# Optimization experiments

Hardware: AMD Instinct MI355X
Metric: run time of the kernel (lower is better)

## Reference

```python
import jax, jax.numpy as jnp
import numpy as np

N = 100000   # nodes
E = 1600000  # edges
D = 128      # input_dim
H = 128      # hidden_dim
O = 64       # output_dim


def setup_inputs() -> dict:
    key = jax.random.key(0)
    ks = jax.random.split(key, 10)
    x = jax.random.normal(ks[0], (N, D), dtype=jnp.float32)
    edge_index = jax.random.randint(ks[1], (2, E), 0, N, dtype=jnp.int32)

    def glorot(k, fan_in, fan_out):
        lim = np.sqrt(6.0 / (fan_in + fan_out)).astype(np.float32)
        return jax.random.uniform(k, (fan_in, fan_out), jnp.float32, -lim, lim)

    return {
        "x": x,
        "edge_index": edge_index,
        "W0": glorot(ks[2], D, H), "b0": jnp.zeros((H,), jnp.float32),
        "W1": glorot(ks[3], H, H), "b1": jnp.zeros((H,), jnp.float32),
        "W2": glorot(ks[4], H, H), "b2": jnp.zeros((H,), jnp.float32),
        "W3": glorot(ks[5], H, O), "b3": jnp.zeros((O,), jnp.float32),
    }


def gcn_conv(x, src, dst, W, b):
    """PyG GCNConv: out = D^{-1/2} (A + I) D^{-1/2} (x W) + b."""
    n = x.shape[0]
    h = x @ W                                # [N, out]
    loop = jnp.arange(n, dtype=src.dtype)    # self loops
    s = jnp.concatenate([src, loop])
    d = jnp.concatenate([dst, loop])
    deg = jax.ops.segment_sum(jnp.ones_like(d, dtype=h.dtype), d, num_segments=n)
    dinv = jax.lax.rsqrt(jnp.maximum(deg, 1.0))  # deg >= 1 because of self loops
    norm = dinv[s] * dinv[d]                     # [E+N]
    out = jax.ops.segment_sum(h[s] * norm[:, None], d, num_segments=n)
    return out + b


def reference(x, edge_index, W0, b0, W1, b1, W2, b2, W3, b3):
    src, dst = edge_index[0], edge_index[1]
    # three GCNBlocks: GCNConv + ReLU (dropout disabled)
    h = jax.nn.relu(gcn_conv(x, src, dst, W0, b0))
    h = jax.nn.relu(gcn_conv(h, src, dst, W1, b1))
    h = jax.nn.relu(gcn_conv(h, src, dst, W2, b2))
    # final bare GCNConv -> output_dim (no activation)
    return gcn_conv(h, src, dst, W3, b3)
```

## Files before the change

### kernel.cpp

```cpp
#include <hip/hip_runtime.h>
#include <math.h>

#define NN 100000
#define NE 1600000
#define NB 391

typedef __attribute__((ext_vector_type(8))) short short8;
typedef __attribute__((ext_vector_type(4))) float f32x4;
union frag8 { short s[8]; short8 v; };

__device__ __forceinline__ void split_bf16(float a, short& hi, short& lo) {
    unsigned u = __float_as_uint(a);
    unsigned hb = u & 0xffff0000u;
    hi = (short)(hb >> 16);
    float r = a - __uint_as_float(hb);
    unsigned lu = __float_as_uint(r);
    lo = (short)((lu + 0x7fff + ((lu >> 16) & 1)) >> 16);
}

__global__ __launch_bounds__(256) void hist_k(const int* __restrict__ dst, int* __restrict__ hist, int e) {
    __shared__ int h[NB];
    int t = threadIdx.x;
    for (int i = t; i < NB; i += 256) h[i] = 0;
    __syncthreads();
    int base = blockIdx.x * 4096;
#pragma unroll
    for (int j = 0; j < 16; ++j) {
        int i = base + j * 256 + t;
        if (i < e) atomicAdd(&h[dst[i] >> 8], 1);
    }
    __syncthreads();
    for (int i = t; i < NB; i += 256) if (h[i]) atomicAdd(&hist[i], h[i]);
}

__global__ __launch_bounds__(512) void bktscan_k(const int* __restrict__ hist,
                                                 int* __restrict__ boff, int* __restrict__ bcur) {
    __shared__ int wsum[8];
    int t = threadIdx.x, lane = t & 63, wid = t >> 6;
    int v = (t < NB) ? hist[t] : 0;
    int inc = v;
#pragma unroll
    for (int off = 1; off < 64; off <<= 1) {
        int tt = __shfl_up(inc, off);
        if (lane >= off) inc += tt;
    }
    if (lane == 63) wsum[wid] = inc;
    __syncthreads();
    int woff = 0;
    for (int w = 0; w < wid; ++w) woff += wsum[w];
    int excl = inc - v + woff;
    if (t < NB) { boff[t] = excl; bcur[t] = excl; }
    if (t == NB - 1) boff[NB] = excl + v;
}

__global__ __launch_bounds__(256) void part2_k(const int* __restrict__ src, const int* __restrict__ dst,
                                               int* bcur, int2* __restrict__ pairs, int e) {
    __shared__ int lhist[NB];
    __shared__ int lbase[NB];
    int t = threadIdx.x;
    for (int i = t; i < NB; i += 256) lhist[i] = 0;
    __syncthreads();
    int e0 = blockIdx.x * 4096;
    int sreg[16], dreg[16];
#pragma unroll
    for (int j = 0; j < 16; ++j) {
        int i = e0 + j * 256 + t;
        if (i < e) {
            sreg[j] = src[i];
            dreg[j] = dst[i];
            atomicAdd(&lhist[dreg[j] >> 8], 1);
        } else dreg[j] = -1;
    }
    __syncthreads();
    for (int i = t; i < NB; i += 256) {
        int c = lhist[i];
        lbase[i] = c ? atomicAdd(&bcur[i], c) : 0;
        lhist[i] = 0;
    }
    __syncthreads();
#pragma unroll
    for (int j = 0; j < 16; ++j) {
        if (dreg[j] >= 0) {
            int b = dreg[j] >> 8;
            int pos = lbase[b] + atomicAdd(&lhist[b], 1);
            pairs[pos] = make_int2(sreg[j], dreg[j]);
        }
    }
}

__global__ __launch_bounds__(256) void cnt2_k(const int2* __restrict__ pairs, const int* __restrict__ boff,
                                              float* __restrict__ dinv, int* __restrict__ rowptr, int n) {
    __shared__ int cnt[256];
    __shared__ int wsum[4];
    int b = blockIdx.x, t = threadIdx.x;
    cnt[t] = 0;
    __syncthreads();
    int e0 = boff[b], e1 = boff[b + 1];
    for (int e = e0 + t; e < e1; e += 256) atomicAdd(&cnt[pairs[e].y & 255], 1);
    __syncthreads();
    int c = cnt[t];
    int lane = t & 63, wid = t >> 6;
    int inc = c;
#pragma unroll
    for (int off = 1; off < 64; off <<= 1) {
        int tt = __shfl_up(inc, off);
        if (lane >= off) inc += tt;
    }
    if (lane == 63) wsum[wid] = inc;
    __syncthreads();
    int woff = 0;
    for (int w = 0; w < wid; ++w) woff += wsum[w];
    int excl = inc - c + woff + e0;
    int i = (b << 8) + t;
    if (i < n) {
        rowptr[i] = excl;
        dinv[i] = 1.0f / sqrtf((float)(c + 1));
    }
    if (b == NB - 1 && t == 255) rowptr[n] = e1;
}

__global__ __launch_bounds__(256) void csrfill_k(const int2* __restrict__ pairs, const int* __restrict__ boff,
                                                 const int* __restrict__ rowptr, int* __restrict__ csr_src, int n) {
    __shared__ int lcur[256];
    int b = blockIdx.x, t = threadIdx.x;
    int i = (b << 8) + t;
    lcur[t] = (i < n) ? rowptr[i] : 0;
    __syncthreads();
    int e0 = boff[b], e1 = boff[b + 1];
    for (int e = e0 + t; e < e1; e += 256) {
        int2 p = pairs[e];
        int pos = atomicAdd(&lcur[p.y & 255], 1);
        csr_src[pos] = p.x;
    }
}

__global__ __launch_bounds__(256) void convw_k(const float* __restrict__ W0, const float* __restrict__ W1,
                                               const float* __restrict__ W2, const float* __restrict__ W3,
                                               short* __restrict__ wt) {
    int gid = blockIdx.x * 256 + threadIdx.x;
    if (gid >= 57344) return;
    const float* W;
    int elem, Ncols, hi_base;
    if (gid < 49152) {
        int w = gid >> 14;
        elem = gid & 16383;
        Ncols = 128;
        W = (w == 0) ? W0 : (w == 1) ? W1 : W2;
        hi_base = w * 32768;
    } else {
        elem = gid - 49152;
        Ncols = 64;
        W = W3;
        hi_base = 98304;
    }
    int k = elem / Ncols, ncol = elem % Ncols;
    short hi, lo;
    split_bf16(W[elem], hi, lo);
    int dstidx = ncol * 128 + k;
    wt[hi_base + dstidx] = hi;
    wt[hi_base + Ncols * 128 + dstidx] = lo;
}

__global__ __launch_bounds__(256) void mfma_gemm_k(const float* __restrict__ A,
                                                   const short* __restrict__ wt_hi,
                                                   const short* __restrict__ wt_lo,
                                                   const float* __restrict__ dinv,
                                                   float* __restrict__ C, int n) {
    constexpr int NT = 8;
    const int tid = threadIdx.x;
    const int wid = tid >> 6, lane = tid & 63;
    const int arow = blockIdx.x * 64 + wid * 16 + (lane & 15);
    const int khalf = lane >> 4;

    f32x4 acc[NT];
#pragma unroll
    for (int nt = 0; nt < NT; ++nt) acc[nt] = (f32x4){0.f, 0.f, 0.f, 0.f};

#pragma unroll
    for (int kc = 0; kc < 4; ++kc) {
        const int k0 = kc * 32 + khalf * 8;
        float4 a0 = make_float4(0.f, 0.f, 0.f, 0.f), a1 = a0;
        if (arow < n) {
            a0 = *(const float4*)(A + (size_t)arow * 128 + k0);
            a1 = *(const float4*)(A + (size_t)arow * 128 + k0 + 4);
        }
        frag8 ahi, alo;
        float av[8] = {a0.x, a0.y, a0.z, a0.w, a1.x, a1.y, a1.z, a1.w};
#pragma unroll
        for (int j = 0; j < 8; ++j) split_bf16(av[j], ahi.s[j], alo.s[j]);

#pragma unroll
        for (int nt = 0; nt < NT; ++nt) {
            const size_t bidx = (size_t)(nt * 16 + (lane & 15)) * 128 + k0;
            short8 bhi = *(const short8*)(wt_hi + bidx);
            short8 blo = *(const short8*)(wt_lo + bidx);
            acc[nt] = __builtin_amdgcn_mfma_f32_16x16x32_bf16(alo.v, bhi, acc[nt], 0, 0, 0);
            acc[nt] = __builtin_amdgcn_mfma_f32_16x16x32_bf16(ahi.v, blo, acc[nt], 0, 0, 0);
            acc[nt] = __builtin_amdgcn_mfma_f32_16x16x32_bf16(ahi.v, bhi, acc[nt], 0, 0, 0);
        }
    }

    const int rbase = blockIdx.x * 64 + wid * 16 + khalf * 4;
    const int col = lane & 15;
    float dv[4];
#pragma unroll
    for (int r = 0; r < 4; ++r) dv[r] = (rbase + r < n) ? dinv[rbase + r] : 0.f;
#pragma unroll
    for (int nt = 0; nt < NT; ++nt) {
#pragma unroll
        for (int r = 0; r < 4; ++r) {
            int row = rbase + r;
            if (row < n) C[(size_t)row * 128 + nt * 16 + col] = acc[nt][r] * dv[r];
        }
    }
}

template<int HOUT>
__global__ __launch_bounds__(256) void fused_k(const float* __restrict__ tmp,
                                               const int* __restrict__ csr_src,
                                               const int* __restrict__ rowptr,
                                               const float* __restrict__ dinv,
                                               const float* __restrict__ bias,
                                               const short* __restrict__ wt_hi,
                                               const short* __restrict__ wt_lo,
                                               float* __restrict__ C, int n) {
    constexpr int NT = HOUT / 32;
    __shared__ float As[32][132];
    const int t = threadIdx.x;
    const int row0 = blockIdx.x * 32;

    {
        const int l = t & 31;
        const int sub = t >> 5;
        float4 bb = *(const float4*)(bias + l * 4);
#pragma unroll
        for (int it = 0; it < 4; ++it) {
            int node = row0 + it * 8 + sub;
            float4 acc = make_float4(0.f, 0.f, 0.f, 0.f);
            if (node < n) {
                float dn = dinv[node];
                acc = *(const float4*)(tmp + (size_t)node * 128 + l * 4);
                int e = rowptr[node];
                const int end = rowptr[node + 1];
                while (e < end) {
                    int m = end - e;
                    if (m > 32) m = 32;
                    int myidx = (e + l < end) ? csr_src[e + l] : 0;
                    int j = 0;
                    for (; j + 4 <= m; j += 4) {
                        int s0 = __shfl(myidx, j, 32);
                        int s1 = __shfl(myidx, j + 1, 32);
                        int s2 = __shfl(myidx, j + 2, 32);
                        int s3 = __shfl(myidx, j + 3, 32);
                        float4 v0 = *(const float4*)(tmp + (size_t)s0 * 128 + l * 4);
                        float4 v1 = *(const float4*)(tmp + (size_t)s1 * 128 + l * 4);
                        float4 v2 = *(const float4*)(tmp + (size_t)s2 * 128 + l * 4);
                        float4 v3 = *(const float4*)(tmp + (size_t)s3 * 128 + l * 4);
                        acc.x += (v0.x + v1.x) + (v2.x + v3.x);
                        acc.y += (v0.y + v1.y) + (v2.y + v3.y);
                        acc.z += (v0.z + v1.z) + (v2.z + v3.z);
                        acc.w += (v0.w + v1.w) + (v2.w + v3.w);
                    }
                    for (; j < m; ++j) {
                        int s0 = __shfl(myidx, j, 32);
                        float4 v0 = *(const float4*)(tmp + (size_t)s0 * 128 + l * 4);
                        acc.x += v0.x; acc.y += v0.y; acc.z += v0.z; acc.w += v0.w;
                    }
                    e += m;
                }
                acc.x = fmaxf(fmaf(acc.x, dn, bb.x), 0.f);
                acc.y = fmaxf(fmaf(acc.y, dn, bb.y), 0.f);
                acc.z = fmaxf(fmaf(acc.z, dn, bb.z), 0.f);
                acc.w = fmaxf(fmaf(acc.w, dn, bb.w), 0.f);
            }
            *(float4*)&As[it * 8 + sub][l * 4] = acc;
        }
    }
    __syncthreads();

    const int wid = t >> 6, lane = t & 63;
    const int rt = wid & 1;
    const int cg = wid >> 1;
    const int arow_l = rt * 16 + (lane & 15);
    const int khalf = lane >> 4;

    f32x4 acc[NT];
#pragma unroll
    for (int nt = 0; nt < NT; ++nt) acc[nt] = (f32x4){0.f, 0.f, 0.f, 0.f};

#pragma unroll
    for (int kc = 0; kc < 4; ++kc) {
        const int k0 = kc * 32 + khalf * 8;
        float4 a0 = *(const float4*)&As[arow_l][k0];
        float4 a1 = *(const float4*)&As[arow_l][k0 + 4];
        frag8 ahi, alo;
        float av[8] = {a0.x, a0.y, a0.z, a0.w, a1.x, a1.y, a1.z, a1.w};
#pragma unroll
        for (int j = 0; j < 8; ++j) split_bf16(av[j], ahi.s[j], alo.s[j]);

#pragma unroll
        for (int nt = 0; nt < NT; ++nt) {
            const size_t bidx = (size_t)(cg * NT * 16 + nt * 16 + (lane & 15)) * 128 + k0;
            short8 bhi = *(const short8*)(wt_hi + bidx);
            short8 blo = *(const short8*)(wt_lo + bidx);
            acc[nt] = __builtin_amdgcn_mfma_f32_16x16x32_bf16(alo.v, bhi, acc[nt], 0, 0, 0);
            acc[nt] = __builtin_amdgcn_mfma_f32_16x16x32_bf16(ahi.v, blo, acc[nt], 0, 0, 0);
            acc[nt] = __builtin_amdgcn_mfma_f32_16x16x32_bf16(ahi.v, bhi, acc[nt], 0, 0, 0);
        }
    }

    const int rbase = row0 + rt * 16 + khalf * 4;
    const int col = lane & 15;
    float dv[4];
#pragma unroll
    for (int r = 0; r < 4; ++r) dv[r] = (rbase + r < n) ? dinv[rbase + r] : 0.f;
#pragma unroll
    for (int nt = 0; nt < NT; ++nt) {
#pragma unroll
        for (int r = 0; r < 4; ++r) {
            int row = rbase + r;
            if (row < n) C[(size_t)row * HOUT + cg * NT * 16 + nt * 16 + col] = acc[nt][r] * dv[r];
        }
    }
}

template<int HOUT>
__global__ __launch_bounds__(256) void agg2_k(const float* __restrict__ tmp,
                                              const int* __restrict__ csr_src,
                                              const int* __restrict__ rowptr,
                                              const float* __restrict__ dinv,
                                              const float* __restrict__ bias,
                                              float* __restrict__ out, int n) {
    constexpr int LPN = HOUT / 4;
    int gid = blockIdx.x * 256 + threadIdx.x;
    int node = gid / LPN, l = gid % LPN;
    if (node >= n) return;

    const float dn = dinv[node];
    float4 bb = *(const float4*)(bias + l * 4);
    float4 acc = *(const float4*)(tmp + (size_t)node * HOUT + l * 4);

    int e = rowptr[node];
    const int end = rowptr[node + 1];
    while (e < end) {
        int m = end - e;
        if (m > LPN) m = LPN;
        int myidx = (e + l < end) ? csr_src[e + l] : 0;
        int j = 0;
        for (; j + 4 <= m; j += 4) {
            int s0 = __shfl(myidx, j, LPN);
            int s1 = __shfl(myidx, j + 1, LPN);
            int s2 = __shfl(myidx, j + 2, LPN);
            int s3 = __shfl(myidx, j + 3, LPN);
            float4 v0 = *(const float4*)(tmp + (size_t)s0 * HOUT + l * 4);
            float4 v1 = *(const float4*)(tmp + (size_t)s1 * HOUT + l * 4);
            float4 v2 = *(const float4*)(tmp + (size_t)s2 * HOUT + l * 4);
            float4 v3 = *(const float4*)(tmp + (size_t)s3 * HOUT + l * 4);
            acc.x += (v0.x + v1.x) + (v2.x + v3.x);
            acc.y += (v0.y + v1.y) + (v2.y + v3.y);
            acc.z += (v0.z + v1.z) + (v2.z + v3.z);
            acc.w += (v0.w + v1.w) + (v2.w + v3.w);
        }
        for (; j < m; ++j) {
            int s0 = __shfl(myidx, j, LPN);
            float4 v0 = *(const float4*)(tmp + (size_t)s0 * HOUT + l * 4);
            acc.x += v0.x; acc.y += v0.y; acc.z += v0.z; acc.w += v0.w;
        }
        e += m;
    }
    float4 o;
    o.x = fmaf(acc.x, dn, bb.x);
    o.y = fmaf(acc.y, dn, bb.y);
    o.z = fmaf(acc.z, dn, bb.z);
    o.w = fmaf(acc.w, dn, bb.w);
    *(float4*)(out + (size_t)node * HOUT + l * 4) = o;
}

extern "C" void kernel_launch(void* const* d_in, const int* in_sizes, int n_in,
                              void* d_out, int out_size, void* d_ws, size_t ws_size,
                              hipStream_t stream) {
    const float* x    = (const float*)d_in[0];
    const int*   ei   = (const int*)d_in[1];
    const int*   srcp = ei;
    const int*   dstp = ei + NE;
    const float* W0 = (const float*)d_in[2]; const float* b0 = (const float*)d_in[3];
    const float* W1 = (const float*)d_in[4]; const float* b1 = (const float*)d_in[5];
    const float* W2 = (const float*)d_in[6]; const float* b2 = (const float*)d_in[7];
    const float* W3 = (const float*)d_in[8]; const float* b3 = (const float*)d_in[9];
    float* out = (float*)d_out;

    char* ws = (char*)d_ws;
    size_t off = 0;
    auto alloc = [&](size_t bytes) { void* p = ws + off; off = (off + bytes + 255) & ~(size_t)255; return p; };
    int*   hist    = (int*)alloc((size_t)NB * 4);
    int*   boff    = (int*)alloc((size_t)(NB + 1) * 4);
    int*   bcur    = (int*)alloc((size_t)NB * 4);
    float* dinv    = (float*)alloc((size_t)NN * 4);
    int*   rowptr  = (int*)alloc((size_t)(NN + 1) * 4);
    int*   csr_src = (int*)alloc((size_t)NE * 4);
    short* wt      = (short*)alloc((size_t)114688 * 2);
    float* bufA    = (float*)alloc((size_t)NN * 128 * 4);
    float* bufB    = (float*)alloc((size_t)NN * 128 * 4);
    int2*  pairs   = (int2*)bufA;

    const int nblk_e4k  = (NE + 4095) / 4096;
    const int nblk_g    = (NN + 63) / 64;
    const int nblk_f    = (NN + 31) / 32;
    const int nblk_a64  = (int)(((size_t)NN * 16 + 255) / 256);

    hipMemsetAsync(hist, 0, (size_t)NB * 4, stream);
    hist_k<<<nblk_e4k, 256, 0, stream>>>(dstp, hist, NE);
    bktscan_k<<<1, 512, 0, stream>>>(hist, boff, bcur);
    part2_k<<<nblk_e4k, 256, 0, stream>>>(srcp, dstp, bcur, pairs, NE);
    cnt2_k<<<NB, 256, 0, stream>>>(pairs, boff, dinv, rowptr, NN);
    csrfill_k<<<NB, 256, 0, stream>>>(pairs, boff, rowptr, csr_src, NN);
    convw_k<<<(57344 + 255) / 256, 256, 0, stream>>>(W0, W1, W2, W3, wt);

    const short* w0h = wt,          *w0l = wt + 16384;
    const short* w1h = wt + 32768,  *w1l = wt + 49152;
    const short* w2h = wt + 65536,  *w2l = wt + 81920;
    const short* w3h = wt + 98304,  *w3l = wt + 106496;

    mfma_gemm_k<<<nblk_g, 256, 0, stream>>>(x, w0h, w0l, dinv, bufB, NN);
    fused_k<128><<<nblk_f, 256, 0, stream>>>(bufB, csr_src, rowptr, dinv, b0, w1h, w1l, bufA, NN);
    fused_k<128><<<nblk_f, 256, 0, stream>>>(bufA, csr_src, rowptr, dinv, b1, w2h, w2l, bufB, NN);
    fused_k<64><<<nblk_f, 256, 0, stream>>>(bufB, csr_src, rowptr, dinv, b2, w3h, w3l, bufA, NN);
    agg2_k<64><<<nblk_a64, 256, 0, stream>>>(bufA, csr_src, rowptr, dinv, b3, out, NN);
}
```

Measured before the change: 634.5 us.

## Merge CSR count/fill kernels, balance gather via node counter, unroll gathers by eight

Combines the degree-count and CSR-fill kernels into one launch by reusing the in-block exclusive scan as the fill cursor, which removes one kernel launch and one pass over rowptr. In the fused aggregation+GEMM kernel, each 32-lane group now takes nodes dynamically from a shared atomic counter instead of a fixed assignment, to balance degree skew within a block. Both gather loops also gain an 8-way unrolled path so more independent row loads are in flight. In exchange the kernel does extra shared atomics and shuffles per node, and the wider unroll uses more registers.

```diff
diff --git a/kernel.cpp b/kernel.cpp
--- a/kernel.cpp
+++ b/kernel.cpp
@@ -88,10 +88,12 @@
     }
 }
 
-__global__ __launch_bounds__(256) void cnt2_k(const int2* __restrict__ pairs, const int* __restrict__ boff,
-                                              float* __restrict__ dinv, int* __restrict__ rowptr, int n) {
+__global__ __launch_bounds__(256) void csr_k(const int2* __restrict__ pairs, const int* __restrict__ boff,
+                                             float* __restrict__ dinv, int* __restrict__ rowptr,
+                                             int* __restrict__ csr_src, int n) {
     __shared__ int cnt[256];
     __shared__ int wsum[4];
+    __shared__ int lcur[256];
     int b = blockIdx.x, t = threadIdx.x;
     cnt[t] = 0;
     __syncthreads();
@@ -117,16 +119,8 @@
         dinv[i] = 1.0f / sqrtf((float)(c + 1));
     }
     if (b == NB - 1 && t == 255) rowptr[n] = e1;
-}
-
-__global__ __launch_bounds__(256) void csrfill_k(const int2* __restrict__ pairs, const int* __restrict__ boff,
-                                                 const int* __restrict__ rowptr, int* __restrict__ csr_src, int n) {
-    __shared__ int lcur[256];
-    int b = blockIdx.x, t = threadIdx.x;
-    int i = (b << 8) + t;
-    lcur[t] = (i < n) ? rowptr[i] : 0;
-    __syncthreads();
-    int e0 = boff[b], e1 = boff[b + 1];
+    lcur[t] = excl;
+    __syncthreads();
     for (int e = e0 + t; e < e1; e += 256) {
         int2 p = pairs[e];
         int pos = atomicAdd(&lcur[p.y & 255], 1);
@@ -226,16 +220,21 @@
                                                float* __restrict__ C, int n) {
     constexpr int NT = HOUT / 32;
     __shared__ float As[32][132];
+    __shared__ int node_ctr;
     const int t = threadIdx.x;
     const int row0 = blockIdx.x * 32;
 
     {
         const int l = t & 31;
-        const int sub = t >> 5;
+        if (t == 0) node_ctr = 0;
+        __syncthreads();
         float4 bb = *(const float4*)(bias + l * 4);
-#pragma unroll
-        for (int it = 0; it < 4; ++it) {
-            int node = row0 + it * 8 + sub;
+        for (;;) {
+            int my = 0;
+            if (l == 0) my = atomicAdd(&node_ctr, 1);
+            my = __shfl(my, 0, 32);
+            if (my >= 32) break;
+            int node = row0 + my;
             float4 acc = make_float4(0.f, 0.f, 0.f, 0.f);
             if (node < n) {
                 float dn = dinv[node];
@@ -247,6 +246,28 @@
                     if (m > 32) m = 32;
                     int myidx = (e + l < end) ? csr_src[e + l] : 0;
                     int j = 0;
+                    for (; j + 8 <= m; j += 8) {
+                        int s0 = __shfl(myidx, j, 32);
+                        int s1 = __shfl(myidx, j + 1, 32);
+                        int s2 = __shfl(myidx, j + 2, 32);
+                        int s3 = __shfl(myidx, j + 3, 32);
+                        int s4 = __shfl(myidx, j + 4, 32);
+                        int s5 = __shfl(myidx, j + 5, 32);
+                        int s6 = __shfl(myidx, j + 6, 32);
+                        int s7 = __shfl(myidx, j + 7, 32);
+                        float4 v0 = *(const float4*)(tmp + (size_t)s0 * 128 + l * 4);
+                        float4 v1 = *(const float4*)(tmp + (size_t)s1 * 128 + l * 4);
+                        float4 v2 = *(const float4*)(tmp + (size_t)s2 * 128 + l * 4);
+                        float4 v3 = *(const float4*)(tmp + (size_t)s3 * 128 + l * 4);
+                        float4 v4 = *(const float4*)(tmp + (size_t)s4 * 128 + l * 4);
+                        float4 v5 = *(const float4*)(tmp + (size_t)s5 * 128 + l * 4);
+                        float4 v6 = *(const float4*)(tmp + (size_t)s6 * 128 + l * 4);
+                        float4 v7 = *(const float4*)(tmp + (size_t)s7 * 128 + l * 4);
+                        acc.x += ((v0.x + v1.x) + (v2.x + v3.x)) + ((v4.x + v5.x) + (v6.x + v7.x));
+                        acc.y += ((v0.y + v1.y) + (v2.y + v3.y)) + ((v4.y + v5.y) + (v6.y + v7.y));
+                        acc.z += ((v0.z + v1.z) + (v2.z + v3.z)) + ((v4.z + v5.z) + (v6.z + v7.z));
+                        acc.w += ((v0.w + v1.w) + (v2.w + v3.w)) + ((v4.w + v5.w) + (v6.w + v7.w));
+                    }
                     for (; j + 4 <= m; j += 4) {
                         int s0 = __shfl(myidx, j, 32);
                         int s1 = __shfl(myidx, j + 1, 32);
@@ -273,7 +294,7 @@
                 acc.z = fmaxf(fmaf(acc.z, dn, bb.z), 0.f);
                 acc.w = fmaxf(fmaf(acc.w, dn, bb.w), 0.f);
             }
-            *(float4*)&As[it * 8 + sub][l * 4] = acc;
+            *(float4*)&As[my][l * 4] = acc;
         }
     }
     __syncthreads();
@@ -347,6 +368,28 @@
         if (m > LPN) m = LPN;
         int myidx = (e + l < end) ? csr_src[e + l] : 0;
         int j = 0;
+        for (; j + 8 <= m; j += 8) {
+            int s0 = __shfl(myidx, j, LPN);
+            int s1 = __shfl(myidx, j + 1, LPN);
+            int s2 = __shfl(myidx, j + 2, LPN);
+            int s3 = __shfl(myidx, j + 3, LPN);
+            int s4 = __shfl(myidx, j + 4, LPN);
+            int s5 = __shfl(myidx, j + 5, LPN);
+            int s6 = __shfl(myidx, j + 6, LPN);
+            int s7 = __shfl(myidx, j + 7, LPN);
+            float4 v0 = *(const float4*)(tmp + (size_t)s0 * HOUT + l * 4);
+            float4 v1 = *(const float4*)(tmp + (size_t)s1 * HOUT + l * 4);
+            float4 v2 = *(const float4*)(tmp + (size_t)s2 * HOUT + l * 4);
+            float4 v3 = *(const float4*)(tmp + (size_t)s3 * HOUT + l * 4);
+            float4 v4 = *(const float4*)(tmp + (size_t)s4 * HOUT + l * 4);
+            float4 v5 = *(const float4*)(tmp + (size_t)s5 * HOUT + l * 4);
+            float4 v6 = *(const float4*)(tmp + (size_t)s6 * HOUT + l * 4);
+            float4 v7 = *(const float4*)(tmp + (size_t)s7 * HOUT + l * 4);
+            acc.x += ((v0.x + v1.x) + (v2.x + v3.x)) + ((v4.x + v5.x) + (v6.x + v7.x));
+            acc.y += ((v0.y + v1.y) + (v2.y + v3.y)) + ((v4.y + v5.y) + (v6.y + v7.y));
+            acc.z += ((v0.z + v1.z) + (v2.z + v3.z)) + ((v4.z + v5.z) + (v6.z + v7.z));
+            acc.w += ((v0.w + v1.w) + (v2.w + v3.w)) + ((v4.w + v5.w) + (v6.w + v7.w));
+        }
         for (; j + 4 <= m; j += 4) {
             int s0 = __shfl(myidx, j, LPN);
             int s1 = __shfl(myidx, j + 1, LPN);
@@ -412,8 +455,7 @@
     hist_k<<<nblk_e4k, 256, 0, stream>>>(dstp, hist, NE);
     bktscan_k<<<1, 512, 0, stream>>>(hist, boff, bcur);
     part2_k<<<nblk_e4k, 256, 0, stream>>>(srcp, dstp, bcur, pairs, NE);
-    cnt2_k<<<NB, 256, 0, stream>>>(pairs, boff, dinv, rowptr, NN);
-    csrfill_k<<<NB, 256, 0, stream>>>(pairs, boff, rowptr, csr_src, NN);
+    csr_k<<<NB, 256, 0, stream>>>(pairs, boff, dinv, rowptr, csr_src, NN);
     convw_k<<<(57344 + 255) / 256, 256, 0, stream>>>(W0, W1, W2, W3, wt);
 
     const short* w0h = wt,          *w0l = wt + 16384;
```

Result: slower. 655.5 us (+3.3%).
